# Optimization experiments

Measured on AMD Instinct MI355X. Metric: run time of the kernel, lower is better.

Reference implementation:

```python
import jax, jax.numpy as jnp
import numpy as np

ALPHA = 0.2
BN_EPS = 1e-5
NEG = -9e15


def make_quaternion_mul(kernel):
    # kernel: [in/4, out]; split columns into quaternion components
    dim = kernel.shape[1] // 4
    r, i, j, k = jnp.split(kernel, 4, axis=1)
    r2 = jnp.concatenate([r, -i, -j, -k], axis=0)
    i2 = jnp.concatenate([i, r, -k, j], axis=0)
    j2 = jnp.concatenate([j, k, r, -i], axis=0)
    k2 = jnp.concatenate([k, -j, i, r], axis=0)
    return jnp.concatenate([r2, i2, j2, k2], axis=1)  # [in, out]


def setup_inputs() -> dict:
    key = jax.random.key(0)
    k1, k2, k3, k4 = jax.random.split(key, 4)
    N, IN, OUT = 8192, 512, 128
    inp = jax.random.normal(k1, (N, IN), dtype=jnp.float32)
    adj = jax.random.randint(k2, (N, N), 0, 2, dtype=jnp.int32)
    # xavier-like init for params
    W = jax.random.normal(k3, (IN // 4, OUT), dtype=jnp.float32) * (1.0 / np.sqrt(IN // 4))
    a = jax.random.normal(k4, (2 * OUT, 1), dtype=jnp.float32) * (1.0 / np.sqrt(2 * OUT))
    bn_gamma = jnp.ones((OUT,), dtype=jnp.float32)
    bn_beta = jnp.zeros((OUT,), dtype=jnp.float32)
    return {"input": inp, "adj": adj, "W": W, "a": a, "bn_gamma": bn_gamma, "bn_beta": bn_beta}


def reference(input, adj, W, a, bn_gamma, bn_beta):
    out_features = W.shape[1]
    hamilton = make_quaternion_mul(W)           # [in, out]
    h = input @ hamilton                        # [N, out]
    # a_input[i,j] = concat(h_i, h_j); a_input @ a decomposes as
    # (h @ a1)_i + (h @ a2)_j with a1 = a[:out], a2 = a[out:]
    a1 = a[:out_features, 0]                    # [out]
    a2 = a[out_features:, 0]                    # [out]
    s1 = h @ a1                                 # [N]
    s2 = h @ a2                                 # [N]
    e = s1[:, None] + s2[None, :]               # [N, N]
    e = jnp.where(e > 0, e, ALPHA * e)          # leaky_relu
    attention = jnp.where(adj > 0, e, NEG)
    attention = jax.nn.softmax(attention, axis=1)
    # dropout is identity in inference
    h_prime = attention @ h                     # [N, out]
    # BatchNorm1d (training-mode batch statistics, biased variance)
    mean = jnp.mean(h_prime, axis=0)
    var = jnp.var(h_prime, axis=0)
    h_prime = (h_prime - mean) / jnp.sqrt(var + BN_EPS) * bn_gamma + bn_beta
    # concat=True -> ELU
    return jax.nn.elu(h_prime)
```

## Files before the change

### kernel.cpp

```cpp
#include <hip/hip_runtime.h>
#include <hip/hip_bf16.h>
#include <math.h>

#define N_NODES 8192
#define IN_F    512
#define OUT_F   128
#define LRELU_A 0.2f
#define EPS_BN  1e-5f
#define MSH     40.0f
#define NSPLIT  8
#define JSPAN   (N_NODES / NSPLIT)
#define TILE_I  64

typedef unsigned short u16;
typedef unsigned int   u32;
typedef unsigned long long u64;
typedef __attribute__((ext_vector_type(8))) short  short8;
typedef __attribute__((ext_vector_type(4))) float  floatx4;

__device__ __forceinline__ u16 f2bf_rtn(float x) {
    u32 u = __float_as_uint(x);
    return (u16)((u + 0x7fffu + ((u >> 16) & 1u)) >> 16);
}

__global__ __launch_bounds__(256) void k_hamT(const float* __restrict__ W, u16* __restrict__ hamT,
                                              float* __restrict__ s1, float* __restrict__ s2,
                                              float* __restrict__ cs, float* __restrict__ cq) {
    const int idx = blockIdx.x * 256 + threadIdx.x;
    if (idx < N_NODES) { s1[idx] = 0.f; s2[idx] = 0.f; }
    if (idx < OUT_F)   { cs[idx] = 0.f; cq[idx] = 0.f; }
    const int c = idx >> 9, k = idx & 511;
    const int b = c >> 5, cc = c & 31, p = k >> 7, q = k & 127;
    const u32 NEGMASK = 0x284Eu;
    const float sg = ((NEGMASK >> (b * 4 + p)) & 1u) ? -1.f : 1.f;
    hamT[idx] = f2bf_rtn(sg * W[q * 128 + (b ^ p) * 32 + cc]);
}

__global__ __launch_bounds__(256) void k_h(const float* __restrict__ inp, const u16* __restrict__ hamT,
                                           const float* __restrict__ a,
                                           u16* __restrict__ hT, float* __restrict__ s1, float* __restrict__ s2) {
    __shared__ float red[4][128][20];
    const int t = threadIdx.x;
    const int lane = t & 63, wid = t >> 6;
    const int quad = lane >> 4, n = lane & 15;
    const int i0 = blockIdx.x * 16;
    const int kb = wid * 128;

    floatx4 acc[8];
#pragma unroll
    for (int ct = 0; ct < 8; ++ct) acc[ct] = (floatx4){0.f, 0.f, 0.f, 0.f};

#pragma unroll
    for (int ks = 0; ks < 4; ++ks) {
        const float* ap = inp + (size_t)(i0 + n) * IN_F + kb + ks * 32 + quad * 8;
        float4 a0 = *(const float4*)ap;
        float4 a1 = *(const float4*)(ap + 4);
        union { u32 u[4]; short8 s; } fa;
        fa.u[0] = (u32)f2bf_rtn(a0.x) | ((u32)f2bf_rtn(a0.y) << 16);
        fa.u[1] = (u32)f2bf_rtn(a0.z) | ((u32)f2bf_rtn(a0.w) << 16);
        fa.u[2] = (u32)f2bf_rtn(a1.x) | ((u32)f2bf_rtn(a1.y) << 16);
        fa.u[3] = (u32)f2bf_rtn(a1.z) | ((u32)f2bf_rtn(a1.w) << 16);
#pragma unroll
        for (int ct = 0; ct < 8; ++ct) {
            short8 fb = *(const short8*)&hamT[(ct * 16 + n) * IN_F + kb + ks * 32 + quad * 8];
            acc[ct] = __builtin_amdgcn_mfma_f32_16x16x32_bf16(fa.s, fb, acc[ct], 0, 0, 0);
        }
    }

    {
        float p1[4] = {0.f, 0.f, 0.f, 0.f}, p2[4] = {0.f, 0.f, 0.f, 0.f};
#pragma unroll
        for (int ct = 0; ct < 8; ++ct) {
            const int c = ct * 16 + n;
            const float a1v = a[c], a2v = a[OUT_F + c];
#pragma unroll
            for (int r = 0; r < 4; ++r) { p1[r] += acc[ct][r] * a1v; p2[r] += acc[ct][r] * a2v; }
        }
#pragma unroll
        for (int m = 1; m < 16; m <<= 1) {
#pragma unroll
            for (int r = 0; r < 4; ++r) {
                p1[r] += __shfl_xor(p1[r], m, 64);
                p2[r] += __shfl_xor(p2[r], m, 64);
            }
        }
        if (n == 0) {
#pragma unroll
            for (int r = 0; r < 4; ++r) {
                atomicAdd(&s1[i0 + quad * 4 + r], p1[r]);
                atomicAdd(&s2[i0 + quad * 4 + r], p2[r]);
            }
        }
    }

#pragma unroll
    for (int ct = 0; ct < 8; ++ct)
        *(float4*)&red[wid][ct * 16 + n][quad * 4] = *(float4*)&acc[ct];
    __syncthreads();

    {
        const int c = t >> 1, ih = (t & 1) * 8;
        float v[8];
#pragma unroll
        for (int e = 0; e < 8; ++e)
            v[e] = red[0][c][ih + e] + red[1][c][ih + e] + red[2][c][ih + e] + red[3][c][ih + e];
        uint4 pk;
        pk.x = (u32)f2bf_rtn(v[0]) | ((u32)f2bf_rtn(v[1]) << 16);
        pk.y = (u32)f2bf_rtn(v[2]) | ((u32)f2bf_rtn(v[3]) << 16);
        pk.z = (u32)f2bf_rtn(v[4]) | ((u32)f2bf_rtn(v[5]) << 16);
        pk.w = (u32)f2bf_rtn(v[6]) | ((u32)f2bf_rtn(v[7]) << 16);
        *(uint4*)&hT[(size_t)c * N_NODES + i0 + ih] = pk;
    }
}

__global__ __launch_bounds__(256, 4) void k_att(const int* __restrict__ adj, const u16* __restrict__ hT,
                                                const float* __restrict__ s1, const float* __restrict__ s2,
                                                float* __restrict__ Opart, float* __restrict__ Lpart) {
    __shared__ u16 hs[2][128 * 64];
    const int t = threadIdx.x;
    const int lane = t & 63, wid = t >> 6;
    const int quad = lane >> 4, n = lane & 15;
    const int i0 = blockIdx.x * TILE_I;
    const int jbase = blockIdx.y * JSPAN;
    const int i_lane = i0 + wid * 16 + n;
    const float s1v = s1[i_lane];
    const int scr = t >> 3, scj = (t & 7) * 8;

    u32 M[4][8];
#pragma unroll
    for (int g = 0; g < 4; ++g)
#pragma unroll
        for (int w = 0; w < 8; ++w) M[g][w] = 0u;
    {
        const size_t rowbase = (size_t)(i0 + wid * 16);
#pragma unroll 4
        for (int rr = 0; rr < 16; ++rr) {
            const int* ap = adj + (rowbase + rr) * N_NODES + jbase + lane * 4;
            uint4 v[4];
#pragma unroll
            for (int g = 0; g < 4; ++g) v[g] = *(const uint4*)(ap + g * 256);
            const bool kp = (n == rr);
#pragma unroll
            for (int g = 0; g < 4; ++g) {
                u64 c0 = __ballot((int)v[g].x > 0);
                u64 c1 = __ballot((int)v[g].y > 0);
                u64 c2 = __ballot((int)v[g].z > 0);
                u64 c3 = __ballot((int)v[g].w > 0);
                if (kp) {
                    M[g][0] = (u32)c0; M[g][1] = (u32)(c0 >> 32);
                    M[g][2] = (u32)c1; M[g][3] = (u32)(c1 >> 32);
                    M[g][4] = (u32)c2; M[g][5] = (u32)(c2 >> 32);
                    M[g][6] = (u32)c3; M[g][7] = (u32)(c3 >> 32);
                }
            }
        }
    }

#pragma unroll
    for (int ps = 0; ps < 4; ++ps) {
        const int cr = ps * 32 + scr;
        uint4 v = *(const uint4*)&hT[(size_t)cr * N_NODES + jbase + scj];
        *(uint4*)&hs[0][cr * 64 + (scj ^ ((cr & 7) * 8))] = v;
    }
    __syncthreads();

    floatx4 acc[8];
#pragma unroll
    for (int ct = 0; ct < 8; ct++) acc[ct] = (floatx4){0.f, 0.f, 0.f, 0.f};
    float Lacc = 0.f;

#pragma unroll
    for (int g = 0; g < 4; ++g) {
#pragma unroll
        for (int chi = 0; chi < 4; ++chi) {
            const int ch = g * 4 + chi;
            const int cur = ch & 1;
            const bool more = (ch + 1 < 16);
            uint4 H[4];
            if (more) {
#pragma unroll
                for (int ps = 0; ps < 4; ++ps) {
                    const int cr = ps * 32 + scr;
                    H[ps] = *(const uint4*)&hT[(size_t)cr * N_NODES + jbase + (ch + 1) * 64 + scj];
                }
            }
            short8 fa[2];
#pragma unroll
            for (int ks = 0; ks < 2; ++ks) {
                const float* s2p = s2 + jbase + ch * 64 + ks * 32 + quad * 8;
                float4 sa = *(const float4*)s2p;
                float4 sb = *(const float4*)(s2p + 4);
                const float sv[8] = {sa.x, sa.y, sa.z, sa.w, sb.x, sb.y, sb.z, sb.w};
                union { u32 u[4]; short8 s; } cv;
#pragma unroll
                for (int jh = 0; jh < 4; ++jh) {
                    float w2[2];
#pragma unroll
                    for (int e = 0; e < 2; ++e) {
                        const int jj = jh * 2 + e;
                        const u32 word = M[g][(jj & 3) * 2 + (chi >> 1)];
                        const int sh = (chi & 1) * 16 + ks * 8 + quad * 2 + (jj >> 2);
                        const u32 mbit = (word >> sh) & 1u;
                        float sc = s1v + sv[jj];
                        sc = fmaxf(sc, LRELU_A * sc);
                        float w = mbit ? __expf(sc - MSH) : 0.f;
                        Lacc += w;
                        w2[e] = w;
                    }
                    cv.u[jh] = (u32)f2bf_rtn(w2[0]) | ((u32)f2bf_rtn(w2[1]) << 16);
                }
                fa[ks] = cv.s;
            }
#pragma unroll
            for (int ct = 0; ct < 8; ++ct) {
                const int rb = ct * 16 + n;
                const int sw = (rb & 7) * 8;
                short8 fb0 = *(const short8*)&hs[cur][rb * 64 + ((quad * 8) ^ sw)];
                short8 fb1 = *(const short8*)&hs[cur][rb * 64 + ((32 + quad * 8) ^ sw)];
                acc[ct] = __builtin_amdgcn_mfma_f32_16x16x32_bf16(fa[0], fb0, acc[ct], 0, 0, 0);
                acc[ct] = __builtin_amdgcn_mfma_f32_16x16x32_bf16(fa[1], fb1, acc[ct], 0, 0, 0);
            }
            if (more) {
#pragma unroll
                for (int ps = 0; ps < 4; ++ps) {
                    const int cr = ps * 32 + scr;
                    *(uint4*)&hs[cur ^ 1][cr * 64 + (scj ^ ((cr & 7) * 8))] = H[ps];
                }
            }
            __syncthreads();
        }
    }

    Lacc += __shfl_xor(Lacc, 16, 64);
    Lacc += __shfl_xor(Lacc, 32, 64);
    if (lane < 16)
        Lpart[(size_t)blockIdx.y * N_NODES + i_lane] = Lacc;

    const size_t obase = (size_t)blockIdx.y * N_NODES * OUT_F;
#pragma unroll
    for (int ct = 0; ct < 8; ++ct) {
#pragma unroll
        for (int r = 0; r < 4; ++r) {
            const int i = i0 + wid * 16 + quad * 4 + r;
            Opart[obase + (size_t)i * OUT_F + ct * 16 + n] = acc[ct][r];
        }
    }
}

__global__ __launch_bounds__(256) void k_comb(const float* __restrict__ Opart, const float* __restrict__ Lpart,
                                              float* __restrict__ hp, float* __restrict__ cs, float* __restrict__ cq) {
    const int t = threadIdx.x;
    const int c = t & 127, half = t >> 7;
    const int ibase = blockIdx.x * 16;
    float sv = 0.f, sq = 0.f;
    for (int k = 0; k < 8; k++) {
        const int i = ibase + half + (k << 1);
        float o = 0.f, L = 0.f;
#pragma unroll
        for (int s = 0; s < NSPLIT; s++) {
            o += Opart[((size_t)s * N_NODES + i) * OUT_F + c];
            L += Lpart[(size_t)s * N_NODES + i];
        }
        float v = L > 0.f ? o / L : 0.f;
        hp[(size_t)i * OUT_F + c] = v;
        sv += v; sq += v * v;
    }
    __shared__ float red[256];
    red[t] = sv; __syncthreads();
    if (half == 0) atomicAdd(&cs[c], sv + red[t + 128]);
    __syncthreads(); red[t] = sq; __syncthreads();
    if (half == 0) atomicAdd(&cq[c], sq + red[t + 128]);
}

__global__ __launch_bounds__(256) void k_bn(const float* __restrict__ hp, const float* __restrict__ cs,
                                            const float* __restrict__ cq, const float* __restrict__ gamma,
                                            const float* __restrict__ beta, float* __restrict__ out) {
    const int idx = blockIdx.x * 256 + threadIdx.x;
    const int c = idx & 127;
    const float mean = cs[c] * (1.f / N_NODES);
    const float var  = cq[c] * (1.f / N_NODES) - mean * mean;
    float x = (hp[idx] - mean) * rsqrtf(var + EPS_BN) * gamma[c] + beta[c];
    x = x > 0.f ? x : expm1f(x);
    out[idx] = x;
}

extern "C" void kernel_launch(void* const* d_in, const int* in_sizes, int n_in,
                              void* d_out, int out_size, void* d_ws, size_t ws_size,
                              hipStream_t stream) {
    (void)in_sizes; (void)n_in; (void)out_size; (void)ws_size;
    const float* inp   = (const float*)d_in[0];
    const int*   adj   = (const int*)d_in[1];
    const float* W     = (const float*)d_in[2];
    const float* a     = (const float*)d_in[3];
    const float* gamma = (const float*)d_in[4];
    const float* beta  = (const float*)d_in[5];
    float* out = (float*)d_out;

    char* wsb = (char*)d_ws;
    u16*   hamT = (u16*)wsb;   wsb += (size_t)OUT_F * IN_F * 2;
    u16*   hT   = (u16*)wsb;   wsb += (size_t)OUT_F * N_NODES * 2;
    float* s1   = (float*)wsb; wsb += N_NODES * 4;
    float* s2   = (float*)wsb; wsb += N_NODES * 4;
    float* Op   = (float*)wsb; wsb += (size_t)NSPLIT * N_NODES * OUT_F * 4;
    float* Lp   = (float*)wsb; wsb += (size_t)NSPLIT * N_NODES * 4;
    float* hp   = (float*)wsb; wsb += (size_t)N_NODES * OUT_F * 4;
    float* cs   = (float*)wsb; wsb += OUT_F * 4;
    float* cq   = (float*)wsb; wsb += OUT_F * 4;

    hipLaunchKernelGGL(k_hamT, dim3(256), dim3(256), 0, stream, W, hamT, s1, s2, cs, cq);
    hipLaunchKernelGGL(k_h,    dim3(512), dim3(256), 0, stream, inp, hamT, a, hT, s1, s2);
    hipLaunchKernelGGL(k_att,  dim3(128, NSPLIT), dim3(256), 0, stream, adj, hT, s1, s2, Op, Lp);
    hipLaunchKernelGGL(k_comb, dim3(512), dim3(256), 0, stream, Op, Lp, hp, cs, cq);
    hipLaunchKernelGGL(k_bn,   dim3(4096), dim3(256), 0, stream, hp, cs, cq, gamma, beta, out);
}
```

Baseline: 455.0 us.

## Pack adjacency into bitmask in separate kernel; stage mask and s2 in LDS

Adds a k_pack kernel that reads the int32 adjacency once and writes a per-row bitmask. The attention kernel then loads only its compact mask slice into shared memory, instead of ballot-packing adjacency rows inside k_att with 15 of 16 ballots discarded per lane. s2 is also staged in LDS, and the XOR swizzle for the h tile is replaced by a padded row stride. The chunk loop is rolled with mask words reloaded from LDS every four chunks, and occupancy drops from 4 to 3 blocks per SM. The cost is an extra launch and a mask round-trip through global memory.

Measured after the change: 492.8 us. 8.3% more time.

```diff
diff --git a/kernel.cpp b/kernel.cpp
--- a/kernel.cpp
+++ b/kernel.cpp
@@ -11,6 +11,8 @@
 #define NSPLIT  8
 #define JSPAN   (N_NODES / NSPLIT)
 #define TILE_I  64
+#define HSTR    72
+#define MSTR    36
 
 typedef unsigned short u16;
 typedef unsigned int   u32;
@@ -36,6 +38,32 @@
     hamT[idx] = f2bf_rtn(sg * W[q * 128 + (b ^ p) * 32 + cc]);
 }
 
+__global__ __launch_bounds__(256) void k_pack(const int* __restrict__ adj, u32* __restrict__ mkg) {
+    const int t = threadIdx.x;
+    const int lane = t & 63, wid = t >> 6;
+    const int row = blockIdx.x * 4 + wid;
+    const int* ar = adj + (size_t)row * N_NODES;
+    u32* mr = mkg + (size_t)row * 256;
+#pragma unroll 2
+    for (int s = 0; s < NSPLIT; ++s) {
+        uint4 v[4];
+#pragma unroll
+        for (int g = 0; g < 4; ++g) v[g] = *(const uint4*)(ar + s * JSPAN + g * 256 + lane * 4);
+        u32* mp = mr + s * 32;
+#pragma unroll
+        for (int g = 0; g < 4; ++g) {
+            u64 c0 = __ballot((int)v[g].x > 0);
+            u64 c1 = __ballot((int)v[g].y > 0);
+            u64 c2 = __ballot((int)v[g].z > 0);
+            u64 c3 = __ballot((int)v[g].w > 0);
+            if (lane < 4) {
+                u64 val = (lane == 0) ? c0 : (lane == 1) ? c1 : (lane == 2) ? c2 : c3;
+                *(u64*)&mp[g * 8 + lane * 2] = val;
+            }
+        }
+    }
+}
+
 __global__ __launch_bounds__(256) void k_h(const float* __restrict__ inp, const u16* __restrict__ hamT,
                                            const float* __restrict__ a,
                                            u16* __restrict__ hT, float* __restrict__ s1, float* __restrict__ s2) {
@@ -113,10 +141,12 @@
     }
 }
 
-__global__ __launch_bounds__(256, 4) void k_att(const int* __restrict__ adj, const u16* __restrict__ hT,
+__global__ __launch_bounds__(256, 3) void k_att(const u32* __restrict__ mkg, const u16* __restrict__ hT,
                                                 const float* __restrict__ s1, const float* __restrict__ s2,
                                                 float* __restrict__ Opart, float* __restrict__ Lpart) {
-    __shared__ u16 hs[2][128 * 64];
+    __shared__ u16 hs[2][128 * HSTR];
+    __shared__ float s2s[JSPAN];
+    __shared__ u32 mk[64 * MSTR];
     const int t = threadIdx.x;
     const int lane = t & 63, wid = t >> 6;
     const int quad = lane >> 4, n = lane & 15;
@@ -126,109 +156,103 @@
     const float s1v = s1[i_lane];
     const int scr = t >> 3, scj = (t & 7) * 8;
 
-    u32 M[4][8];
-#pragma unroll
-    for (int g = 0; g < 4; ++g)
-#pragma unroll
-        for (int w = 0; w < 8; ++w) M[g][w] = 0u;
+    *(float4*)&s2s[t * 4] = *(const float4*)&s2[jbase + t * 4];
+
     {
-        const size_t rowbase = (size_t)(i0 + wid * 16);
-#pragma unroll 4
-        for (int rr = 0; rr < 16; ++rr) {
-            const int* ap = adj + (rowbase + rr) * N_NODES + jbase + lane * 4;
-            uint4 v[4];
-#pragma unroll
-            for (int g = 0; g < 4; ++g) v[g] = *(const uint4*)(ap + g * 256);
-            const bool kp = (n == rr);
-#pragma unroll
-            for (int g = 0; g < 4; ++g) {
-                u64 c0 = __ballot((int)v[g].x > 0);
-                u64 c1 = __ballot((int)v[g].y > 0);
-                u64 c2 = __ballot((int)v[g].z > 0);
-                u64 c3 = __ballot((int)v[g].w > 0);
-                if (kp) {
-                    M[g][0] = (u32)c0; M[g][1] = (u32)(c0 >> 32);
-                    M[g][2] = (u32)c1; M[g][3] = (u32)(c1 >> 32);
-                    M[g][4] = (u32)c2; M[g][5] = (u32)(c2 >> 32);
-                    M[g][6] = (u32)c3; M[g][7] = (u32)(c3 >> 32);
-                }
-            }
-        }
+        const int rl = t >> 2, wo = (t & 3) * 8;
+        const u32* gp = mkg + (size_t)(i0 + rl) * 256 + blockIdx.y * 32 + wo;
+        uint4 a0 = *(const uint4*)gp;
+        uint4 a1 = *(const uint4*)(gp + 4);
+        *(uint4*)&mk[rl * MSTR + wo]     = a0;
+        *(uint4*)&mk[rl * MSTR + wo + 4] = a1;
     }
 
 #pragma unroll
     for (int ps = 0; ps < 4; ++ps) {
         const int cr = ps * 32 + scr;
         uint4 v = *(const uint4*)&hT[(size_t)cr * N_NODES + jbase + scj];
-        *(uint4*)&hs[0][cr * 64 + (scj ^ ((cr & 7) * 8))] = v;
+        *(uint4*)&hs[0][cr * HSTR + scj] = v;
     }
     __syncthreads();
+
+    u32 m8[8];
+    {
+        const u32* mp = &mk[(wid * 16 + n) * MSTR];
+#pragma unroll
+        for (int w = 0; w < 8; ++w) m8[w] = mp[w];
+    }
 
     floatx4 acc[8];
 #pragma unroll
     for (int ct = 0; ct < 8; ct++) acc[ct] = (floatx4){0.f, 0.f, 0.f, 0.f};
     float Lacc = 0.f;
 
-#pragma unroll
-    for (int g = 0; g < 4; ++g) {
-#pragma unroll
-        for (int chi = 0; chi < 4; ++chi) {
-            const int ch = g * 4 + chi;
-            const int cur = ch & 1;
-            const bool more = (ch + 1 < 16);
-            uint4 H[4];
-            if (more) {
-#pragma unroll
-                for (int ps = 0; ps < 4; ++ps) {
-                    const int cr = ps * 32 + scr;
-                    H[ps] = *(const uint4*)&hT[(size_t)cr * N_NODES + jbase + (ch + 1) * 64 + scj];
+#pragma unroll 4
+    for (int ch = 0; ch < 16; ++ch) {
+        const int cur = ch & 1;
+        const bool more = (ch + 1 < 16);
+        uint4 H[4];
+        if (more) {
+#pragma unroll
+            for (int ps = 0; ps < 4; ++ps) {
+                const int cr = ps * 32 + scr;
+                H[ps] = *(const uint4*)&hT[(size_t)cr * N_NODES + jbase + (ch + 1) * 64 + scj];
+            }
+        }
+        u32 m8n[8];
+#pragma unroll
+        for (int w = 0; w < 8; ++w) m8n[w] = m8[w];
+        if ((ch & 3) == 3 && more) {
+            const u32* mp = &mk[(wid * 16 + n) * MSTR + ((ch >> 2) + 1) * 8];
+#pragma unroll
+            for (int w = 0; w < 8; ++w) m8n[w] = mp[w];
+        }
+
+        short8 fa[2];
+#pragma unroll
+        for (int ks = 0; ks < 2; ++ks) {
+            const int jl = ch * 64 + ks * 32 + quad * 8;
+            float4 sa = *(const float4*)&s2s[jl];
+            float4 sb = *(const float4*)&s2s[jl + 4];
+            const float sv[8] = {sa.x, sa.y, sa.z, sa.w, sb.x, sb.y, sb.z, sb.w};
+            union { u32 u[4]; short8 s; } cv;
+#pragma unroll
+            for (int jh = 0; jh < 4; ++jh) {
+                float w2[2];
+#pragma unroll
+                for (int e = 0; e < 2; ++e) {
+                    const int jj = jh * 2 + e;
+                    const u32 word = m8[(jj & 3) * 2 + ((ch >> 1) & 1)];
+                    const int sh = (ch & 1) * 16 + ks * 8 + quad * 2 + (jj >> 2);
+                    const u32 mbit = (word >> sh) & 1u;
+                    float sc = s1v + sv[jj];
+                    sc = fmaxf(sc, LRELU_A * sc);
+                    float w = mbit ? __expf(sc - MSH) : 0.f;
+                    Lacc += w;
+                    w2[e] = w;
                 }
-            }
-            short8 fa[2];
-#pragma unroll
-            for (int ks = 0; ks < 2; ++ks) {
-                const float* s2p = s2 + jbase + ch * 64 + ks * 32 + quad * 8;
-                float4 sa = *(const float4*)s2p;
-                float4 sb = *(const float4*)(s2p + 4);
-                const float sv[8] = {sa.x, sa.y, sa.z, sa.w, sb.x, sb.y, sb.z, sb.w};
-                union { u32 u[4]; short8 s; } cv;
-#pragma unroll
-                for (int jh = 0; jh < 4; ++jh) {
-                    float w2[2];
-#pragma unroll
-                    for (int e = 0; e < 2; ++e) {
-                        const int jj = jh * 2 + e;
-                        const u32 word = M[g][(jj & 3) * 2 + (chi >> 1)];
-                        const int sh = (chi & 1) * 16 + ks * 8 + quad * 2 + (jj >> 2);
-                        const u32 mbit = (word >> sh) & 1u;
-                        float sc = s1v + sv[jj];
-                        sc = fmaxf(sc, LRELU_A * sc);
-                        float w = mbit ? __expf(sc - MSH) : 0.f;
-                        Lacc += w;
-                        w2[e] = w;
-                    }
-                    cv.u[jh] = (u32)f2bf_rtn(w2[0]) | ((u32)f2bf_rtn(w2[1]) << 16);
-                }
-                fa[ks] = cv.s;
-            }
-#pragma unroll
-            for (int ct = 0; ct < 8; ++ct) {
-                const int rb = ct * 16 + n;
-                const int sw = (rb & 7) * 8;
-                short8 fb0 = *(const short8*)&hs[cur][rb * 64 + ((quad * 8) ^ sw)];
-                short8 fb1 = *(const short8*)&hs[cur][rb * 64 + ((32 + quad * 8) ^ sw)];
-                acc[ct] = __builtin_amdgcn_mfma_f32_16x16x32_bf16(fa[0], fb0, acc[ct], 0, 0, 0);
-                acc[ct] = __builtin_amdgcn_mfma_f32_16x16x32_bf16(fa[1], fb1, acc[ct], 0, 0, 0);
-            }
-            if (more) {
-#pragma unroll
-                for (int ps = 0; ps < 4; ++ps) {
-                    const int cr = ps * 32 + scr;
-                    *(uint4*)&hs[cur ^ 1][cr * 64 + (scj ^ ((cr & 7) * 8))] = H[ps];
-                }
-            }
-            __syncthreads();
-        }
+                cv.u[jh] = (u32)f2bf_rtn(w2[0]) | ((u32)f2bf_rtn(w2[1]) << 16);
+            }
+            fa[ks] = cv.s;
+        }
+#pragma unroll
+        for (int ct = 0; ct < 8; ++ct) {
+            const int boff = (ct * 16 + n) * HSTR;
+            short8 fb0 = *(const short8*)&hs[cur][boff + quad * 8];
+            short8 fb1 = *(const short8*)&hs[cur][boff + 32 + quad * 8];
+            acc[ct] = __builtin_amdgcn_mfma_f32_16x16x32_bf16(fa[0], fb0, acc[ct], 0, 0, 0);
+            acc[ct] = __builtin_amdgcn_mfma_f32_16x16x32_bf16(fa[1], fb1, acc[ct], 0, 0, 0);
+        }
+        if (more) {
+#pragma unroll
+            for (int ps = 0; ps < 4; ++ps) {
+                const int cr = ps * 32 + scr;
+                *(uint4*)&hs[cur ^ 1][cr * HSTR + scj] = H[ps];
+            }
+        }
+        __syncthreads();
+#pragma unroll
+        for (int w = 0; w < 8; ++w) m8[w] = m8n[w];
     }
 
     Lacc += __shfl_xor(Lacc, 16, 64);
@@ -306,10 +330,12 @@
     float* hp   = (float*)wsb; wsb += (size_t)N_NODES * OUT_F * 4;
     float* cs   = (float*)wsb; wsb += OUT_F * 4;
     float* cq   = (float*)wsb; wsb += OUT_F * 4;
+    u32*   mkg  = (u32*)wsb;   wsb += (size_t)N_NODES * 256 * 4;
 
     hipLaunchKernelGGL(k_hamT, dim3(256), dim3(256), 0, stream, W, hamT, s1, s2, cs, cq);
     hipLaunchKernelGGL(k_h,    dim3(512), dim3(256), 0, stream, inp, hamT, a, hT, s1, s2);
-    hipLaunchKernelGGL(k_att,  dim3(128, NSPLIT), dim3(256), 0, stream, adj, hT, s1, s2, Op, Lp);
+    hipLaunchKernelGGL(k_pack, dim3(2048), dim3(256), 0, stream, adj, mkg);
+    hipLaunchKernelGGL(k_att,  dim3(128, NSPLIT), dim3(256), 0, stream, mkg, hT, s1, s2, Op, Lp);
     hipLaunchKernelGGL(k_comb, dim3(512), dim3(256), 0, stream, Op, Lp, hp, cs, cq);
     hipLaunchKernelGGL(k_bn,   dim3(4096), dim3(256), 0, stream, hp, cs, cq, gamma, beta, out);
 }
```
